# Kernel optimization log

Hardware: AMD Instinct MI355X
Metric: run time of the kernel (lower is better)

## Reference

```python
import jax, jax.numpy as jnp
import numpy as np
from jax import lax

B, X, H, W, C = 4, 32, 8, 128, 32  # batch, frames, height, width, channels (dim)


def setup_inputs() -> dict:
    key = jax.random.key(0)
    k1, k2, k3, k4, k5, k6 = jax.random.split(key, 6)
    return {
        "storage": jax.random.normal(k1, (B, X, H, W, C), jnp.float32),
        "target": jax.random.normal(k2, (B, 1, H, W, C), jnp.float32),
        # Conv3d(dim, 2*dim, kernel=(3,1,1), padding=(1,0,0)) weight/bias
        "w_cross": jax.random.normal(k3, (2 * C, C, 3, 1, 1), jnp.float32) * 0.05,
        "b_cross": jax.random.normal(k4, (2 * C,), jnp.float32) * 0.05,
        # Conv2d(dim, dim, kernel=1) weight (stored as [out, in]) / bias
        "w_q": jax.random.normal(k5, (C, C), jnp.float32) * 0.1,
        "b_q": jax.random.normal(k6, (C,), jnp.float32) * 0.1,
    }


def reference(storage, target, w_cross, b_cross, w_q, b_q):
    # storage [B,X,H,W,C] -> transpose(4,1).transpose(4,2) -> [B,C,X,W,H]
    s = jnp.transpose(storage, (0, 4, 1, 3, 2))
    # target [B,1,H,W,C] -> transpose(4,2) -> [B,1,C,W,H] -> squeeze(1) -> [B,C,W,H]
    t = jnp.transpose(target, (0, 1, 4, 3, 2))[:, 0]

    # Conv3d over the X (depth) axis, kernel (3,1,1), padding (1,0,0)
    out = lax.conv_general_dilated(
        s, w_cross, window_strides=(1, 1, 1),
        padding=((1, 1), (0, 0), (0, 0)),
        dimension_numbers=("NCDHW", "OIDHW", "NCDHW"),
    ) + b_cross[None, :, None, None, None]          # [B,2C,X,W,H]
    s_v, s_k = jnp.split(out, 2, axis=1)            # each [B,C,X,W,H]

    # 1x1 Conv2d query projection
    t_q = jnp.einsum("oc,bcwh->bowh", w_q, t) + b_q[None, :, None, None]  # [B,C,W,H]
    # unsqueeze(1).transpose(2,1).repeat over X -> [B,C,X,W,H]
    t_q = jnp.broadcast_to(t_q[:, :, None], (B, C, X, W, H))

    # Faithful torch .view on contiguous [B,C,X,W,H]: row-major reshape mixes C into last dim
    t_q = t_q.reshape(B, X * W, C * H)
    s_v = s_v.reshape(B, X * W, C * H)
    s_k = jnp.swapaxes(s_k.reshape(B, X * W, C * H), 1, 2)  # [B, C*H, X*W]

    kq = jax.nn.softmax(jnp.einsum("bnc,bcm->bnm", t_q, s_k), axis=-1)  # [B, XW, XW]
    final = jnp.einsum("bnm,bmc->bnc", kq, s_v)                          # [B, XW, C*H]
    return final.reshape(B, X, H, W, C)
```

## Files before the change

### kernel.cpp

```cpp
#include <hip/hip_runtime.h>

typedef unsigned short u16;
typedef unsigned int u32;
typedef __attribute__((ext_vector_type(8))) short s16x8;
typedef __attribute__((ext_vector_type(4))) float f32x4;

#define WS_A      0u
#define WS_B      8388608u
#define WS_C      16777216u
#define WS_LP     25452544u
#define WS_NEEDED 25485312u

__device__ __forceinline__ u16 f2bf(float f){
  u32 u = __float_as_uint(f);
  return (u16)((u + 0x7fffu + ((u >> 16) & 1u)) >> 16);
}

__global__ __launch_bounds__(256) void zero_out_kernel(float* __restrict__ out){
  int t = blockIdx.x * 256 + threadIdx.x;
  ((float4*)out)[t] = make_float4(0.f, 0.f, 0.f, 0.f);
}

__global__ __launch_bounds__(256, 4) void conv_kernel(const float* __restrict__ storage,
    const float* __restrict__ w_cross, const float* __restrict__ b_cross,
    u16* __restrict__ Kb, u16* __restrict__ Vb){
  int bid = blockIdx.x;
  int mhalf = bid & 1;
  int wc    = (bid >> 1) & 3;
  int x     = (bid >> 3) & 31;
  int b     = bid >> 8;
  int tid = threadIdx.x;
  int w4 = tid >> 6;
  int lane = tid & 63, l15 = lane & 15, quad = lane >> 4;

  s16x8 Ahi[3], Alo[3];
  {
    int o = w4*16 + l15;
    const float4* wp = (const float4*)(w_cross + o*96 + quad*24);
    float w24[24];
    #pragma unroll
    for (int i = 0; i < 6; ++i){
      float4 v = wp[i];
      w24[i*4+0] = v.x; w24[i*4+1] = v.y; w24[i*4+2] = v.z; w24[i*4+3] = v.w;
    }
    #pragma unroll
    for (int dx = 0; dx < 3; ++dx){
      #pragma unroll
      for (int e = 0; e < 8; ++e){
        float wv = w24[e*3 + dx];
        u32 u = __float_as_uint(wv);
        float r = wv - __uint_as_float(u & 0xffff0000u);
        Ahi[dx][e] = (short)(u >> 16);
        Alo[dx][e] = (short)(__float_as_uint(r) >> 16);
      }
    }
  }

  f32x4 acc[8];
  {
    float4 bv = *(const float4*)(b_cross + w4*16 + quad*4);
    #pragma unroll
    for (int mt = 0; mt < 8; ++mt) acc[mt] = (f32x4){bv.x, bv.y, bv.z, bv.w};
  }

  #pragma unroll
  for (int dx = 0; dx < 3; ++dx){
    int xx = x + dx - 1;
    if (xx < 0 || xx > 31) continue;
    const float* pb = storage +
        ((((size_t)b*32 + xx)*8 + (l15 & 7))*128 + wc*32 + mhalf*16 + (l15 >> 3))*32 + quad*8;
    #pragma unroll
    for (int mt = 0; mt < 8; ++mt){
      float4 va  = *(const float4*)(pb + mt*64);
      float4 vb2 = *(const float4*)(pb + mt*64 + 4);
      float v[8] = {va.x, va.y, va.z, va.w, vb2.x, vb2.y, vb2.z, vb2.w};
      s16x8 bhi, blo;
      #pragma unroll
      for (int e = 0; e < 8; ++e){
        u32 u = __float_as_uint(v[e]);
        float r = v[e] - __uint_as_float(u & 0xffff0000u);
        bhi[e] = (short)(u >> 16);
        blo[e] = (short)(__float_as_uint(r) >> 16);
      }
      acc[mt] = __builtin_amdgcn_mfma_f32_16x16x32_bf16(Ahi[dx], bhi, acc[mt], 0, 0, 0);
      acc[mt] = __builtin_amdgcn_mfma_f32_16x16x32_bf16(Ahi[dx], blo, acc[mt], 0, 0, 0);
      acc[mt] = __builtin_amdgcn_mfma_f32_16x16x32_bf16(Alo[dx], bhi, acc[mt], 0, 0, 0);
    }
  }

  __shared__ u16 st[64 * 128];
  #pragma unroll
  for (int mt = 0; mt < 8; ++mt){
    #pragma unroll
    for (int r = 0; r < 4; ++r)
      st[(w4*16 + quad*4 + r)*128 + mt*16 + l15] = f2bf(acc[mt][r]);
  }
  __syncthreads();
  int o = tid >> 2, part = tid & 3;
  int ck = o & 31;
  size_t base = ((size_t)b*4096 + (size_t)ck*128 + (size_t)x*4 + wc)*256 + mhalf*128 + part*32;
  u16* dst = (o < 32 ? Vb : Kb) + base;
  const u16* src = &st[o*128 + part*32];
  *(uint4*)(dst)      = *(const uint4*)(src);
  *(uint4*)(dst + 8)  = *(const uint4*)(src + 8);
  *(uint4*)(dst + 16) = *(const uint4*)(src + 16);
  *(uint4*)(dst + 24) = *(const uint4*)(src + 24);
}

__global__ __launch_bounds__(256, 2) void flash_kernel(const float* __restrict__ target,
    const float* __restrict__ w_q, const float* __restrict__ b_q,
    const u16* __restrict__ Kb, const u16* __restrict__ Vb,
    float* __restrict__ Opart, float* __restrict__ lpart){
  int kq = blockIdx.x & 15, rb = (blockIdx.x >> 4) & 7, b = blockIdx.x >> 7;
  int tid = threadIdx.x;
  int w = tid >> 6, lane = tid & 63, l15 = lane & 15, quad = lane >> 4;

  __shared__ alignas(16) u16 Vts[256 * 64];
  __shared__ alignas(16) u16 Ps[16 * 64];
  __shared__ float lsumW[64];

  u16* stgQ = Vts;
  {
    int wl = tid & 31, h = tid >> 5;
    #pragma unroll
    for (int wcq = 0; wcq < 4; ++wcq){
      float in[32];
      const float4* p = (const float4*)(target + (((size_t)b*8 + h)*128 + wcq*32 + wl)*32);
      #pragma unroll
      for (int q = 0; q < 8; ++q){
        float4 v = p[q];
        in[q*4+0] = v.x; in[q*4+1] = v.y; in[q*4+2] = v.z; in[q*4+3] = v.w;
      }
      #pragma unroll
      for (int cql = 0; cql < 4; ++cql){
        int cq = rb*4 + cql;
        float acc = b_q[cq];
        #pragma unroll
        for (int c = 0; c < 32; ++c) acc = fmaf(in[c], w_q[cq*32 + c], acc);
        stgQ[(cql*4 + wcq)*264 + wl*8 + h] = f2bf(acc);
      }
    }
  }
  __syncthreads();

  s16x8 qa[8];
  {
    const u16* qp = stgQ + l15*264 + quad*8;
    #pragma unroll
    for (int ks = 0; ks < 8; ++ks) qa[ks] = *(const s16x8*)(qp + ks*32);
  }
  __syncthreads();

  int jl4 = tid & 15, mseg = tid >> 4;
  const u16* kbase = Kb + ((size_t)(b*4096 + kq*256 + w*16 + l15))*256 + quad*8;
  const u16* vbase = Vb + ((size_t)(b*4096 + kq*256 + jl4*4))*256 + mseg*16;

  s16x8 kr[8];
  #pragma unroll
  for (int ks = 0; ks < 8; ++ks) kr[ks] = *(const s16x8*)(kbase + ks*32);
  u32 kv[4][8];
  #pragma unroll
  for (int kk = 0; kk < 4; ++kk){
    uint4 a = *(const uint4*)(vbase + kk*256);
    uint4 b2 = *(const uint4*)(vbase + kk*256 + 8);
    kv[kk][0]=a.x; kv[kk][1]=a.y; kv[kk][2]=a.z; kv[kk][3]=a.w;
    kv[kk][4]=b2.x; kv[kk][5]=b2.y; kv[kk][6]=b2.z; kv[kk][7]=b2.w;
  }

  float lacc[4] = {0.f, 0.f, 0.f, 0.f};
  f32x4 oc[4];
  #pragma unroll
  for (int mt = 0; mt < 4; ++mt) oc[mt] = (f32x4){0.f,0.f,0.f,0.f};

  #pragma unroll
  for (int it = 0; it < 4; ++it){
    if (it > 0) __syncthreads();

    #pragma unroll
    for (int i = 0; i < 16; ++i){
      int d = i >> 1;
      u32 e0, e1, e2, e3;
      if (i & 1){ e0 = kv[0][d] >> 16;     e1 = kv[1][d] >> 16;
                  e2 = kv[2][d] >> 16;     e3 = kv[3][d] >> 16; }
      else      { e0 = kv[0][d] & 0xffffu; e1 = kv[1][d] & 0xffffu;
                  e2 = kv[2][d] & 0xffffu; e3 = kv[3][d] & 0xffffu; }
      int m = mseg*16 + i;
      int col = (((jl4 >> 1) ^ (m & 7)) << 3) + ((jl4 & 1) << 2);
      *(uint2*)&Vts[m*64 + col] = make_uint2(e0 | (e1 << 16), e2 | (e3 << 16));
    }

    f32x4 s0 = {0.f,0.f,0.f,0.f}, s1 = {0.f,0.f,0.f,0.f};
    #pragma unroll
    for (int ks = 0; ks < 8; ks += 2){
      s0 = __builtin_amdgcn_mfma_f32_16x16x32_bf16(qa[ks],   kr[ks],   s0, 0, 0, 0);
      s1 = __builtin_amdgcn_mfma_f32_16x16x32_bf16(qa[ks+1], kr[ks+1], s1, 0, 0, 0);
    }
    int b8k = w*2 + (l15 >> 3);
    #pragma unroll
    for (int reg = 0; reg < 4; ++reg){
      float sv = fminf(s0[reg] + s1[reg], 80.f);
      float p = __expf(sv);
      int row = quad*4 + reg;
      Ps[row*64 + ((b8k ^ (row & 7)) << 3) + (l15 & 7)] = f2bf(p);
      lacc[reg] += p;
    }

    if (it < 3){
      const u16* vp = vbase + (it+1)*16384;
      #pragma unroll
      for (int kk = 0; kk < 4; ++kk){
        uint4 a = *(const uint4*)(vp + kk*256);
        uint4 b2 = *(const uint4*)(vp + kk*256 + 8);
        kv[kk][0]=a.x; kv[kk][1]=a.y; kv[kk][2]=a.z; kv[kk][3]=a.w;
        kv[kk][4]=b2.x; kv[kk][5]=b2.y; kv[kk][6]=b2.z; kv[kk][7]=b2.w;
      }
    }
    __syncthreads();

    if (it < 3){
      const u16* kp = kbase + (it+1)*16384;
      #pragma unroll
      for (int ks = 0; ks < 8; ++ks) kr[ks] = *(const s16x8*)(kp + ks*32);
    }
    #pragma unroll
    for (int ks2 = 0; ks2 < 2; ++ks2){
      int b8 = ks2*4 + quad;
      s16x8 pb = *(const s16x8*)&Ps[l15*64 + ((b8 ^ (l15 & 7)) << 3)];
      #pragma unroll
      for (int mt = 0; mt < 4; ++mt){
        int mrow = (w*4 + mt)*16 + l15;
        s16x8 af = *(const s16x8*)&Vts[mrow*64 + ((b8 ^ (mrow & 7)) << 3)];
        oc[mt] = __builtin_amdgcn_mfma_f32_16x16x32_bf16(af, pb, oc[mt], 0, 0, 0);
      }
    }
  }

  #pragma unroll
  for (int reg = 0; reg < 4; ++reg){
    float t = lacc[reg];
    t += __shfl_xor(t, 1); t += __shfl_xor(t, 2);
    t += __shfl_xor(t, 4); t += __shfl_xor(t, 8);
    lacc[reg] = t;
  }
  if (l15 == 0){
    #pragma unroll
    for (int reg = 0; reg < 4; ++reg) lsumW[w*16 + quad*4 + reg] = lacc[reg];
  }
  __syncthreads();
  if (tid < 16)
    lpart[(b*16 + kq)*128 + rb*16 + tid] =
        lsumW[tid] + lsumW[16 + tid] + lsumW[32 + tid] + lsumW[48 + tid];
  {
    float* dst = Opart + ((size_t)((b*16 + kq)*128 + rb*16 + l15))*256 + w*64 + quad*4;
    #pragma unroll
    for (int mt = 0; mt < 4; ++mt)
      *(float4*)(dst + mt*16) = make_float4(oc[mt][0], oc[mt][1], oc[mt][2], oc[mt][3]);
  }
}

__global__ __launch_bounds__(256) void combine_kernel(const float* __restrict__ lpart,
    const float* __restrict__ Opart, float* __restrict__ out){
  int r = blockIdx.x & 127, b = blockIdx.x >> 7;
  int m = threadIdx.x;
  float L = 0.f, o = 0.f;
  #pragma unroll
  for (int kq = 0; kq < 16; ++kq){
    L += lpart[(b*16 + kq)*128 + r];
    o += Opart[((size_t)((b*16 + kq)*128 + r))*256 + m];
  }
  o /= L;
  int cq = r >> 2, whi = r & 3;
  size_t obase = ((size_t)b*32 + cq) * 32768;
  #pragma unroll
  for (int hh = 0; hh < 8; ++hh){
    #pragma unroll
    for (int wt = 0; wt < 4; ++wt){
      out[obase + hh*4096 + wt*1024 + whi*256 + m] = o;
    }
  }
}

extern "C" void kernel_launch(void* const* d_in, const int* in_sizes, int n_in,
                              void* d_out, int out_size, void* d_ws, size_t ws_size,
                              hipStream_t stream){
  const float* storage = (const float*)d_in[0];
  const float* target  = (const float*)d_in[1];
  const float* w_cross = (const float*)d_in[2];
  const float* b_cross = (const float*)d_in[3];
  const float* w_q     = (const float*)d_in[4];
  const float* b_q     = (const float*)d_in[5];
  float* out = (float*)d_out;

  if (ws_size < (size_t)WS_NEEDED){
    zero_out_kernel<<<dim3(4096), dim3(256), 0, stream>>>(out);
    return;
  }

  char* ws = (char*)d_ws;
  float* Opart = (float*)(ws + WS_A);
  u16*   Kb    = (u16*)(ws + WS_B);
  u16*   Vb    = (u16*)(ws + WS_C);
  float* lpart = (float*)(ws + WS_LP);

  conv_kernel    <<<dim3(1024), dim3(256), 0, stream>>>(storage, w_cross, b_cross, Kb, Vb);
  flash_kernel   <<<dim3(512),  dim3(256), 0, stream>>>(target, w_q, b_q, Kb, Vb, Opart, lpart);
  combine_kernel <<<dim3(512),  dim3(256), 0, stream>>>(lpart, Opart, out);
}
```

Measured before the change: 141.8 us.

## Split conv blocks by output-channel half instead of spatial half, batch loads

Each conv block now computes one half of the output channels (V or K) across the full 32-wide spatial tile instead of all 64 outputs over half the width. Block indices are remapped so the eight blocks with consecutive ids cover different regions. Global loads are issued four at a time before the MFMAs to raise memory-level parallelism, and the LDS staging buffer is padded to stride 264 so each block writes contiguous 512-byte rows. The trade-off is that each storage element is now read by two blocks, once for V and once for K.

```diff
diff --git a/kernel.cpp b/kernel.cpp
--- a/kernel.cpp
+++ b/kernel.cpp
@@ -24,18 +24,19 @@
 __global__ __launch_bounds__(256, 4) void conv_kernel(const float* __restrict__ storage,
     const float* __restrict__ w_cross, const float* __restrict__ b_cross,
     u16* __restrict__ Kb, u16* __restrict__ Vb){
-  int bid = blockIdx.x;
-  int mhalf = bid & 1;
-  int wc    = (bid >> 1) & 3;
-  int x     = (bid >> 3) & 31;
-  int b     = bid >> 8;
+  int o_idx = (blockIdx.x & 7) * 128 + (blockIdx.x >> 3);
+  int og2 = o_idx & 1;
+  int wc  = (o_idx >> 1) & 3;
+  int x   = (o_idx >> 3) & 31;
+  int b   = o_idx >> 8;
   int tid = threadIdx.x;
   int w4 = tid >> 6;
+  int oh = w4 >> 1, mh = w4 & 1;
   int lane = tid & 63, l15 = lane & 15, quad = lane >> 4;
 
   s16x8 Ahi[3], Alo[3];
   {
-    int o = w4*16 + l15;
+    int o = og2*32 + oh*16 + l15;
     const float4* wp = (const float4*)(w_cross + o*96 + quad*24);
     float w24[24];
     #pragma unroll
@@ -58,7 +59,7 @@
 
   f32x4 acc[8];
   {
-    float4 bv = *(const float4*)(b_cross + w4*16 + quad*4);
+    float4 bv = *(const float4*)(b_cross + og2*32 + oh*16 + quad*4);
     #pragma unroll
     for (int mt = 0; mt < 8; ++mt) acc[mt] = (f32x4){bv.x, bv.y, bv.z, bv.w};
   }
@@ -68,43 +69,50 @@
     int xx = x + dx - 1;
     if (xx < 0 || xx > 31) continue;
     const float* pb = storage +
-        ((((size_t)b*32 + xx)*8 + (l15 & 7))*128 + wc*32 + mhalf*16 + (l15 >> 3))*32 + quad*8;
-    #pragma unroll
-    for (int mt = 0; mt < 8; ++mt){
-      float4 va  = *(const float4*)(pb + mt*64);
-      float4 vb2 = *(const float4*)(pb + mt*64 + 4);
-      float v[8] = {va.x, va.y, va.z, va.w, vb2.x, vb2.y, vb2.z, vb2.w};
-      s16x8 bhi, blo;
-      #pragma unroll
-      for (int e = 0; e < 8; ++e){
-        u32 u = __float_as_uint(v[e]);
-        float r = v[e] - __uint_as_float(u & 0xffff0000u);
-        bhi[e] = (short)(u >> 16);
-        blo[e] = (short)(__float_as_uint(r) >> 16);
-      }
-      acc[mt] = __builtin_amdgcn_mfma_f32_16x16x32_bf16(Ahi[dx], bhi, acc[mt], 0, 0, 0);
-      acc[mt] = __builtin_amdgcn_mfma_f32_16x16x32_bf16(Ahi[dx], blo, acc[mt], 0, 0, 0);
-      acc[mt] = __builtin_amdgcn_mfma_f32_16x16x32_bf16(Alo[dx], bhi, acc[mt], 0, 0, 0);
-    }
-  }
-
-  __shared__ u16 st[64 * 128];
+        ((((size_t)b*32 + xx)*8 + (l15 & 7))*128 + wc*32 + mh*16 + (l15 >> 3))*32 + quad*8;
+    #pragma unroll
+    for (int g = 0; g < 2; ++g){
+      float4 va[4], vb4[4];
+      #pragma unroll
+      for (int k = 0; k < 4; ++k){
+        va[k]  = *(const float4*)(pb + (g*4 + k)*64);
+        vb4[k] = *(const float4*)(pb + (g*4 + k)*64 + 4);
+      }
+      #pragma unroll
+      for (int k = 0; k < 4; ++k){
+        int mt = g*4 + k;
+        float v[8] = {va[k].x, va[k].y, va[k].z, va[k].w,
+                      vb4[k].x, vb4[k].y, vb4[k].z, vb4[k].w};
+        s16x8 bhi, blo;
+        #pragma unroll
+        for (int e = 0; e < 8; ++e){
+          u32 u = __float_as_uint(v[e]);
+          float r = v[e] - __uint_as_float(u & 0xffff0000u);
+          bhi[e] = (short)(u >> 16);
+          blo[e] = (short)(__float_as_uint(r) >> 16);
+        }
+        acc[mt] = __builtin_amdgcn_mfma_f32_16x16x32_bf16(Ahi[dx], bhi, acc[mt], 0, 0, 0);
+        acc[mt] = __builtin_amdgcn_mfma_f32_16x16x32_bf16(Ahi[dx], blo, acc[mt], 0, 0, 0);
+        acc[mt] = __builtin_amdgcn_mfma_f32_16x16x32_bf16(Alo[dx], bhi, acc[mt], 0, 0, 0);
+      }
+    }
+  }
+
+  __shared__ u16 st[32 * 264];
   #pragma unroll
   for (int mt = 0; mt < 8; ++mt){
     #pragma unroll
     for (int r = 0; r < 4; ++r)
-      st[(w4*16 + quad*4 + r)*128 + mt*16 + l15] = f2bf(acc[mt][r]);
+      st[(oh*16 + quad*4 + r)*264 + mh*128 + mt*16 + l15] = f2bf(acc[mt][r]);
   }
   __syncthreads();
-  int o = tid >> 2, part = tid & 3;
-  int ck = o & 31;
-  size_t base = ((size_t)b*4096 + (size_t)ck*128 + (size_t)x*4 + wc)*256 + mhalf*128 + part*32;
-  u16* dst = (o < 32 ? Vb : Kb) + base;
-  const u16* src = &st[o*128 + part*32];
-  *(uint4*)(dst)      = *(const uint4*)(src);
-  *(uint4*)(dst + 8)  = *(const uint4*)(src + 8);
-  *(uint4*)(dst + 16) = *(const uint4*)(src + 16);
-  *(uint4*)(dst + 24) = *(const uint4*)(src + 24);
+  int o_loc = tid >> 3, part = tid & 7;
+  size_t base = ((size_t)b*4096 + (size_t)o_loc*128 + (size_t)x*4 + wc)*256 + part*8;
+  u16* dst = (og2 == 0 ? Vb : Kb) + base;
+  const u16* src = &st[o_loc*264 + part*8];
+  #pragma unroll
+  for (int i = 0; i < 4; ++i)
+    *(uint4*)(dst + i*64) = *(const uint4*)(src + i*64);
 }
 
 __global__ __launch_bounds__(256, 2) void flash_kernel(const float* __restrict__ target,
```

Result: no change. 139.7 us (-1.5%).
